# Optimization experiments

Measured on AMD Instinct MI355X. Metric: run time of the kernel, lower is better.

The kernel has to match this reference:

```python
import jax, jax.numpy as jnp
import numpy as np

K = 24  # number of clusters (all ids in [0,K) assumed present per image)
DELTA_VAR = 1.0
DELTA_DIST = 2.0
VAR_W = 1.0
DIST_W = 1.0
REG_W = 1.0


def setup_inputs() -> dict:
    key = jax.random.key(0)
    k1, k2 = jax.random.split(key)
    data = jax.random.normal(k1, (4, 16, 512, 1024), dtype=jnp.float32)
    labels = jax.random.randint(k2, (4, 512, 1024), 0, K, dtype=jnp.int32)
    return {"data": data, "labels": labels}


def reference(data, labels):
    B, D, H, Wd = data.shape
    N = H * Wd
    # [B, N, D] points, [B*N] global segment ids (batch-offset cluster ids)
    X = jnp.transpose(data.reshape(B, D, N), (0, 2, 1)).reshape(B * N, D)
    seg = (labels.reshape(B, N) + jnp.arange(B, dtype=labels.dtype)[:, None] * K).reshape(-1)

    # per-cluster sums and counts -> centers  [B*K, D]
    sums = jax.ops.segment_sum(X, seg, num_segments=B * K)
    counts = jax.ops.segment_sum(jnp.ones((B * N,), X.dtype), seg, num_segments=B * K)
    centers_flat = sums / counts[:, None]
    centers = centers_flat.reshape(B, K, D)
    counts_bk = counts.reshape(B, K)

    # variance term: per-point hinged distance to own cluster center
    c_per_point = centers_flat[seg]                      # [B*N, D]
    pt_dist = jnp.linalg.norm(X - c_per_point, axis=1)   # [B*N]
    hv = jnp.maximum(pt_dist - DELTA_VAR, 0.0) ** 2
    var_per_cluster = jax.ops.segment_sum(hv, seg, num_segments=B * K).reshape(B, K) / counts_bk
    var_sum = var_per_cluster.sum()

    # distance term: pairwise center distances (diagonal kept, as in original,
    # contributing a constant delta_dist**2 per cluster)
    diff = centers[:, :, None, :] - centers[:, None, :, :]     # [B, K, K, D]
    sq = jnp.sum(diff * diff, axis=-1)                         # [B, K, K]
    eye = jnp.eye(K, dtype=bool)[None]
    cdist = jnp.where(eye, 0.0, jnp.sqrt(jnp.where(eye, 1.0, sq)))
    hd = jnp.maximum(DELTA_DIST - cdist, 0.0) ** 2
    dist_sum = hd.sum() / (2.0 * K * (K - 1))

    # regularization: mean center norm per image, summed over batch
    reg_sum = jnp.linalg.norm(centers, axis=2).mean(axis=1).sum()

    loss = (VAR_W * var_sum + DIST_W * dist_sum + REG_W * reg_sum) / B
    return loss
```

## Files before the change

kernel.cpp:

```cpp
#include <hip/hip_runtime.h>
#include <math.h>

#define KC 24
constexpr int D = 16;
constexpr int B = 4;
constexpr int N = 512 * 1024;
constexpr float DELTA_VAR = 1.0f;
constexpr float DELTA_DIST = 2.0f;

constexpr int REP = 8;
constexpr int RS  = KC * 17;
constexpr int CS  = 33;
constexpr int PTS = 1024;
constexpr int BLOCKS = (B * N) / PTS;
constexpr int SL = 8;


__global__ __launch_bounds__(256) void k_sums(const float* __restrict__ data,
                                              const int* __restrict__ labels,
                                              float* __restrict__ g_sums,
                                              float* __restrict__ g_cnt) {
    __shared__ float s_sum[REP * RS];
    __shared__ float s_cnt[REP * CS];
    const int t = threadIdx.x;
    for (int i = t; i < REP * RS; i += 256) s_sum[i] = 0.f;
    for (int i = t; i < REP * CS; i += 256) s_cnt[i] = 0.f;
    __syncthreads();

    const int chunk = blockIdx.x * PTS;
    const int b     = chunk >> 19;
    const int n0    = (chunk & (N - 1)) + t * 4;

    const int4 lab = *(const int4*)(labels + chunk + t * 4);
    const int rbase = (t & 7) * RS;
    const int ax = rbase + lab.x * 17;
    const int ay = rbase + lab.y * 17;
    const int az = rbase + lab.z * 17;
    const int aw = rbase + lab.w * 17;

    const float* base = data + (size_t)(b * D) * N + n0;
    float4 v[D];
#pragma unroll
    for (int d = 0; d < D; ++d) v[d] = *(const float4*)(base + (size_t)d * N);

    const int cbase = (t & 7) * CS;
    atomicAdd(&s_cnt[cbase + lab.x], 1.f);
    atomicAdd(&s_cnt[cbase + lab.y], 1.f);
    atomicAdd(&s_cnt[cbase + lab.z], 1.f);
    atomicAdd(&s_cnt[cbase + lab.w], 1.f);

#pragma unroll
    for (int d = 0; d < D; ++d) {
        atomicAdd(&s_sum[ax + d], v[d].x);
        atomicAdd(&s_sum[ay + d], v[d].y);
        atomicAdd(&s_sum[az + d], v[d].z);
        atomicAdd(&s_sum[aw + d], v[d].w);
    }
    __syncthreads();

    const int slice = blockIdx.x & (SL - 1);
    float* gs = g_sums + slice * (B * KC * D) + b * (KC * D);
    float* gc = g_cnt  + slice * (B * KC)     + b * KC;
    const int rot = (blockIdx.x * 131) & 255;
    for (int i = t; i < KC * D; i += 256) {
        int j = (i + rot) % (KC * D);
        int c = j >> 4, d = j & 15;
        float s = 0.f;
#pragma unroll
        for (int r = 0; r < REP; ++r) s += s_sum[r * RS + c * 17 + d];
        atomicAdd(&gs[j], s);
    }
    if (t < KC) {
        float s = 0.f;
#pragma unroll
        for (int r = 0; r < REP; ++r) s += s_cnt[r * CS + t];
        atomicAdd(&gc[t], s);
    }
}

__global__ __launch_bounds__(256) void k_var(const float* __restrict__ data,
                                             const int* __restrict__ labels,
                                             const float* __restrict__ g_sums,
                                             const float* __restrict__ g_cnt,
                                             float* __restrict__ g_varp) {
    __shared__ float s_c[KC * 17];
    __shared__ float s_ic[KC];
    __shared__ float s_part[4];
    const int t = threadIdx.x;
    const int chunk = blockIdx.x * PTS;
    const int b     = chunk >> 19;
    const int n0    = (chunk & (N - 1)) + t * 4;

    if (t < KC) {
        float cn = 0.f;
#pragma unroll
        for (int r = 0; r < SL; ++r) cn += g_cnt[r * (B * KC) + b * KC + t];
        s_ic[t] = 1.f / cn;
    }
    __syncthreads();
    for (int i = t; i < KC * D; i += 256) {
        int c = i >> 4, d = i & 15;
        float s = 0.f;
#pragma unroll
        for (int r = 0; r < SL; ++r) s += g_sums[r * (B * KC * D) + b * (KC * D) + i];
        s_c[c * 17 + d] = s * s_ic[c];
    }
    __syncthreads();

    const int4 lab = *(const int4*)(labels + chunk + t * 4);
    const int ax = lab.x * 17, ay = lab.y * 17, az = lab.z * 17, aw = lab.w * 17;

    const float* base = data + (size_t)(b * D) * N + n0;
    float4 v[D];
#pragma unroll
    for (int d = 0; d < D; ++d) v[d] = *(const float4*)(base + (size_t)d * N);

    float4 acc = {0.f, 0.f, 0.f, 0.f};
#pragma unroll
    for (int d = 0; d < D; ++d) {
        float df;
        df = v[d].x - s_c[ax + d]; acc.x += df * df;
        df = v[d].y - s_c[ay + d]; acc.y += df * df;
        df = v[d].z - s_c[az + d]; acc.z += df * df;
        df = v[d].w - s_c[aw + d]; acc.w += df * df;
    }
    float h, hsum;
    h = fmaxf(sqrtf(acc.x) - DELTA_VAR, 0.f); hsum  = h * h * s_ic[lab.x];
    h = fmaxf(sqrtf(acc.y) - DELTA_VAR, 0.f); hsum += h * h * s_ic[lab.y];
    h = fmaxf(sqrtf(acc.z) - DELTA_VAR, 0.f); hsum += h * h * s_ic[lab.z];
    h = fmaxf(sqrtf(acc.w) - DELTA_VAR, 0.f); hsum += h * h * s_ic[lab.w];

    for (int o = 32; o > 0; o >>= 1) hsum += __shfl_down(hsum, o, 64);
    if ((t & 63) == 0) s_part[t >> 6] = hsum;
    __syncthreads();
    if (t == 0)
        atomicAdd(&g_varp[blockIdx.x & 63],
                  s_part[0] + s_part[1] + s_part[2] + s_part[3]);
}

__global__ __launch_bounds__(128) void k_final(const float* __restrict__ g_sums,
                                               const float* __restrict__ g_cnt,
                                               const float* __restrict__ g_varp,
                                               float* __restrict__ out) {
    __shared__ float s_c[B * KC * 17];
    __shared__ float s_red[2];
    const int t = threadIdx.x;

    float acc = 0.f;
    if (t < B * KC) {
        float cnt = 0.f;
#pragma unroll
        for (int r = 0; r < SL; ++r) cnt += g_cnt[r * (B * KC) + t];
        float ns = 0.f;
        for (int d = 0; d < D; ++d) {
            float s = 0.f;
#pragma unroll
            for (int r = 0; r < SL; ++r) s += g_sums[r * (B * KC * D) + t * D + d];
            float c = s / cnt;
            s_c[t * 17 + d] = c;
            ns += c * c;
        }
        acc = sqrtf(ns) / (float)KC;
    }
    if (t < 64) acc += g_varp[t];
    __syncthreads();

    float dacc = 0.f;
    for (int idx = t; idx < B * KC * KC; idx += 128) {
        int b = idx / (KC * KC);
        int r = idx % (KC * KC);
        int i = r / KC, j = r % KC;
        float hd;
        if (i == j) {
            hd = DELTA_DIST * DELTA_DIST;
        } else {
            const float* ci = &s_c[(b * KC + i) * 17];
            const float* cj = &s_c[(b * KC + j) * 17];
            float sq = 0.f;
            for (int d = 0; d < D; ++d) { float df = ci[d] - cj[d]; sq += df * df; }
            float hh = fmaxf(DELTA_DIST - sqrtf(sq), 0.f);
            hd = hh * hh;
        }
        dacc += hd;
    }
    float total = acc + dacc / (2.f * KC * (KC - 1));

    for (int o = 32; o > 0; o >>= 1) total += __shfl_down(total, o, 64);
    if ((t & 63) == 0) s_red[t >> 6] = total;
    __syncthreads();
    if (t == 0) out[0] = (s_red[0] + s_red[1]) / (float)B;
}

extern "C" void kernel_launch(void* const* d_in, const int* in_sizes, int n_in,
                              void* d_out, int out_size, void* d_ws, size_t ws_size,
                              hipStream_t stream) {
    const float* data  = (const float*)d_in[0];
    const int* labels  = (const int*)d_in[1];
    float* ws = (float*)d_ws;
    float* g_sums = ws;
    float* g_cnt  = g_sums + SL * (B * KC * D);
    float* g_varp = g_cnt  + SL * (B * KC);

    hipMemsetAsync(d_ws, 0,
                   (SL * (B * KC * D) + SL * (B * KC) + 64) * sizeof(float), stream);

    k_sums<<<BLOCKS, 256, 0, stream>>>(data, labels, g_sums, g_cnt);
    k_var <<<BLOCKS, 256, 0, stream>>>(data, labels, g_sums, g_cnt, g_varp);
    k_final<<<1, 128, 0, stream>>>(g_sums, g_cnt, g_varp, (float*)d_out);
}
```

Measured before the change: 364.3 us.

## Process 4096 points per block with double-buffered per-dimension loads

New measurement: 353.1 us. 3.1% less time.

```diff
diff --git a/kernel.cpp b/kernel.cpp
--- a/kernel.cpp
+++ b/kernel.cpp
@@ -11,7 +11,7 @@
 constexpr int REP = 8;
 constexpr int RS  = KC * 17;
 constexpr int CS  = 33;
-constexpr int PTS = 1024;
+constexpr int PTS = 4096;
 constexpr int BLOCKS = (B * N) / PTS;
 constexpr int SL = 8;
 
@@ -23,38 +23,61 @@
     __shared__ float s_sum[REP * RS];
     __shared__ float s_cnt[REP * CS];
     const int t = threadIdx.x;
+
+    const int chunk = blockIdx.x * PTS;
+    const int b     = chunk >> 19;
+    const int n0    = chunk & (N - 1);
+
+    int4 lab[4];
+#pragma unroll
+    for (int i = 0; i < 4; ++i)
+        lab[i] = *(const int4*)(labels + chunk + (i * 256 + t) * 4);
+
+    const float* base = data + (size_t)(b * D) * N + n0;
+    float4 v[2][4];
+#pragma unroll
+    for (int i = 0; i < 4; ++i)
+        v[0][i] = *(const float4*)(base + (i * 256 + t) * 4);
+
     for (int i = t; i < REP * RS; i += 256) s_sum[i] = 0.f;
     for (int i = t; i < REP * CS; i += 256) s_cnt[i] = 0.f;
-    __syncthreads();
-
-    const int chunk = blockIdx.x * PTS;
-    const int b     = chunk >> 19;
-    const int n0    = (chunk & (N - 1)) + t * 4;
-
-    const int4 lab = *(const int4*)(labels + chunk + t * 4);
+
     const int rbase = (t & 7) * RS;
-    const int ax = rbase + lab.x * 17;
-    const int ay = rbase + lab.y * 17;
-    const int az = rbase + lab.z * 17;
-    const int aw = rbase + lab.w * 17;
-
-    const float* base = data + (size_t)(b * D) * N + n0;
-    float4 v[D];
-#pragma unroll
-    for (int d = 0; d < D; ++d) v[d] = *(const float4*)(base + (size_t)d * N);
+    int adr[4][4];
+#pragma unroll
+    for (int i = 0; i < 4; ++i) {
+        adr[i][0] = rbase + lab[i].x * 17;
+        adr[i][1] = rbase + lab[i].y * 17;
+        adr[i][2] = rbase + lab[i].z * 17;
+        adr[i][3] = rbase + lab[i].w * 17;
+    }
+    __syncthreads();
 
     const int cbase = (t & 7) * CS;
-    atomicAdd(&s_cnt[cbase + lab.x], 1.f);
-    atomicAdd(&s_cnt[cbase + lab.y], 1.f);
-    atomicAdd(&s_cnt[cbase + lab.z], 1.f);
-    atomicAdd(&s_cnt[cbase + lab.w], 1.f);
+#pragma unroll
+    for (int i = 0; i < 4; ++i) {
+        atomicAdd(&s_cnt[cbase + lab[i].x], 1.f);
+        atomicAdd(&s_cnt[cbase + lab[i].y], 1.f);
+        atomicAdd(&s_cnt[cbase + lab[i].z], 1.f);
+        atomicAdd(&s_cnt[cbase + lab[i].w], 1.f);
+    }
 
 #pragma unroll
     for (int d = 0; d < D; ++d) {
-        atomicAdd(&s_sum[ax + d], v[d].x);
-        atomicAdd(&s_sum[ay + d], v[d].y);
-        atomicAdd(&s_sum[az + d], v[d].z);
-        atomicAdd(&s_sum[aw + d], v[d].w);
+        if (d < D - 1) {
+#pragma unroll
+            for (int i = 0; i < 4; ++i)
+                v[(d + 1) & 1][i] =
+                    *(const float4*)(base + (size_t)(d + 1) * N + (i * 256 + t) * 4);
+        }
+#pragma unroll
+        for (int i = 0; i < 4; ++i) {
+            const float4 c = v[d & 1][i];
+            atomicAdd(&s_sum[adr[i][0] + d], c.x);
+            atomicAdd(&s_sum[adr[i][1] + d], c.y);
+            atomicAdd(&s_sum[adr[i][2] + d], c.z);
+            atomicAdd(&s_sum[adr[i][3] + d], c.w);
+        }
     }
     __syncthreads();
 
@@ -89,7 +112,18 @@
     const int t = threadIdx.x;
     const int chunk = blockIdx.x * PTS;
     const int b     = chunk >> 19;
-    const int n0    = (chunk & (N - 1)) + t * 4;
+    const int n0    = chunk & (N - 1);
+
+    int4 lab[4];
+#pragma unroll
+    for (int i = 0; i < 4; ++i)
+        lab[i] = *(const int4*)(labels + chunk + (i * 256 + t) * 4);
+
+    const float* base = data + (size_t)(b * D) * N + n0;
+    float4 v[2][4];
+#pragma unroll
+    for (int i = 0; i < 4; ++i)
+        v[0][i] = *(const float4*)(base + (i * 256 + t) * 4);
 
     if (t < KC) {
         float cn = 0.f;
@@ -107,28 +141,47 @@
     }
     __syncthreads();
 
-    const int4 lab = *(const int4*)(labels + chunk + t * 4);
-    const int ax = lab.x * 17, ay = lab.y * 17, az = lab.z * 17, aw = lab.w * 17;
-
-    const float* base = data + (size_t)(b * D) * N + n0;
-    float4 v[D];
-#pragma unroll
-    for (int d = 0; d < D; ++d) v[d] = *(const float4*)(base + (size_t)d * N);
-
-    float4 acc = {0.f, 0.f, 0.f, 0.f};
+    int adr[4][4];
+#pragma unroll
+    for (int i = 0; i < 4; ++i) {
+        adr[i][0] = lab[i].x * 17;
+        adr[i][1] = lab[i].y * 17;
+        adr[i][2] = lab[i].z * 17;
+        adr[i][3] = lab[i].w * 17;
+    }
+
+    float4 acc[4];
+#pragma unroll
+    for (int i = 0; i < 4; ++i) acc[i] = make_float4(0.f, 0.f, 0.f, 0.f);
+
 #pragma unroll
     for (int d = 0; d < D; ++d) {
-        float df;
-        df = v[d].x - s_c[ax + d]; acc.x += df * df;
-        df = v[d].y - s_c[ay + d]; acc.y += df * df;
-        df = v[d].z - s_c[az + d]; acc.z += df * df;
-        df = v[d].w - s_c[aw + d]; acc.w += df * df;
-    }
-    float h, hsum;
-    h = fmaxf(sqrtf(acc.x) - DELTA_VAR, 0.f); hsum  = h * h * s_ic[lab.x];
-    h = fmaxf(sqrtf(acc.y) - DELTA_VAR, 0.f); hsum += h * h * s_ic[lab.y];
-    h = fmaxf(sqrtf(acc.z) - DELTA_VAR, 0.f); hsum += h * h * s_ic[lab.z];
-    h = fmaxf(sqrtf(acc.w) - DELTA_VAR, 0.f); hsum += h * h * s_ic[lab.w];
+        if (d < D - 1) {
+#pragma unroll
+            for (int i = 0; i < 4; ++i)
+                v[(d + 1) & 1][i] =
+                    *(const float4*)(base + (size_t)(d + 1) * N + (i * 256 + t) * 4);
+        }
+#pragma unroll
+        for (int i = 0; i < 4; ++i) {
+            const float4 c = v[d & 1][i];
+            float df;
+            df = c.x - s_c[adr[i][0] + d]; acc[i].x += df * df;
+            df = c.y - s_c[adr[i][1] + d]; acc[i].y += df * df;
+            df = c.z - s_c[adr[i][2] + d]; acc[i].z += df * df;
+            df = c.w - s_c[adr[i][3] + d]; acc[i].w += df * df;
+        }
+    }
+
+    float hsum = 0.f;
+#pragma unroll
+    for (int i = 0; i < 4; ++i) {
+        float h;
+        h = fmaxf(sqrtf(acc[i].x) - DELTA_VAR, 0.f); hsum += h * h * s_ic[lab[i].x];
+        h = fmaxf(sqrtf(acc[i].y) - DELTA_VAR, 0.f); hsum += h * h * s_ic[lab[i].y];
+        h = fmaxf(sqrtf(acc[i].z) - DELTA_VAR, 0.f); hsum += h * h * s_ic[lab[i].z];
+        h = fmaxf(sqrtf(acc[i].w) - DELTA_VAR, 0.f); hsum += h * h * s_ic[lab[i].w];
+    }
 
     for (int o = 32; o > 0; o >>= 1) hsum += __shfl_down(hsum, o, 64);
     if ((t & 63) == 0) s_part[t >> 6] = hsum;
```
